# Optimization experiments

Hardware: AMD Instinct MI355X
Metric: run time of the kernel (lower is better)

## Reference

```python
import jax, jax.numpy as jnp
import numpy as np

N_NODES = 50000
N_GRAPHS = 250
NODES_PER_GRAPH = 200
EDGES_PER_GRAPH = 3200  # avg degree 16
F_IN = 128
EMB = 128
HID = 128
VOCAB = 1000
N_REL = 8


def setup_inputs() -> dict:
    key = jax.random.key(0)
    ks = jax.random.split(key, 16)

    # message: col 0 = discrete token id (stored as float), col 1 = continuous value
    disc = jax.random.randint(ks[0], (N_GRAPHS,), 0, VOCAB).astype(jnp.float32)
    cont = jax.random.normal(ks[1], (N_GRAPHS,), dtype=jnp.float32)
    message = jnp.stack([disc, cont], axis=1)  # [B, 2]

    x = jax.random.normal(ks[2], (N_NODES, F_IN), dtype=jnp.float32)

    # within-graph edges: local indices + per-graph node offset
    offs = (jnp.arange(N_GRAPHS, dtype=jnp.int64) * NODES_PER_GRAPH)[:, None]
    src = (jax.random.randint(ks[3], (N_GRAPHS, EDGES_PER_GRAPH), 0, NODES_PER_GRAPH) + offs).reshape(-1)
    dst = (jax.random.randint(ks[4], (N_GRAPHS, EDGES_PER_GRAPH), 0, NODES_PER_GRAPH) + offs).reshape(-1)
    edge_index = jnp.stack([src, dst], axis=0).astype(jnp.int64)  # [2, E]
    edge_type = jax.random.randint(ks[5], (N_GRAPHS * EDGES_PER_GRAPH,), 0, N_REL).astype(jnp.int64)

    batch = jnp.repeat(jnp.arange(N_GRAPHS, dtype=jnp.int64), NODES_PER_GRAPH)  # [N]

    s = 0.05
    W1 = jax.random.normal(ks[6], (N_REL, F_IN, EMB), dtype=jnp.float32) * s
    root1 = jax.random.normal(ks[7], (F_IN, EMB), dtype=jnp.float32) * s
    b1 = jnp.zeros((EMB,), dtype=jnp.float32)
    W2 = jax.random.normal(ks[8], (N_REL, EMB, EMB), dtype=jnp.float32) * s
    root2 = jax.random.normal(ks[9], (EMB, EMB), dtype=jnp.float32) * s
    b2 = jnp.zeros((EMB,), dtype=jnp.float32)
    embed_table = jax.random.normal(ks[10], (VOCAB, EMB), dtype=jnp.float32) * s
    cont_w = jax.random.normal(ks[11], (1, EMB), dtype=jnp.float32) * s
    cont_b = jnp.zeros((EMB,), dtype=jnp.float32)
    msg_w = jax.random.normal(ks[12], (2 * EMB, HID), dtype=jnp.float32) * s
    msg_b = jnp.zeros((HID,), dtype=jnp.float32)

    return {
        "message": message, "x": x, "edge_index": edge_index, "edge_type": edge_type,
        "batch": batch, "max_nodes": NODES_PER_GRAPH,
        "W1": W1, "root1": root1, "b1": b1, "W2": W2, "root2": root2, "b2": b2,
        "embed_table": embed_table, "cont_w": cont_w, "cont_b": cont_b,
        "msg_w": msg_w, "msg_b": msg_b,
    }


def _rgcn_conv(h, src, dst, edge_type, W, root, b, n_nodes, n_rel):
    # per-node per-relation transform, then gather per edge: avoids [E,F,F] weight gather
    hW = jnp.einsum('nf,rfo->nro', h, W)          # [N, R, O]
    msg = hW[src, edge_type]                       # [E, O]
    # mean aggregation per (dst, relation) as in PyG RGCNConv(aggr='mean')
    key_dr = dst * n_rel + edge_type
    cnt = jax.ops.segment_sum(jnp.ones_like(edge_type, dtype=h.dtype), key_dr,
                              num_segments=n_nodes * n_rel)
    norm = 1.0 / jnp.maximum(cnt[key_dr], 1.0)     # [E]
    agg = jax.ops.segment_sum(msg * norm[:, None], dst, num_segments=n_nodes)  # [N, O]
    return agg + h @ root + b


def reference(message, x, edge_index, edge_type, batch, max_nodes,
              W1, root1, b1, W2, root2, b2,
              embed_table, cont_w, cont_b, msg_w, msg_b):
    n_nodes = x.shape[0]
    n_rel = W1.shape[0]
    n_graphs = message.shape[0]
    src, dst = edge_index[0], edge_index[1]

    # --- RGCN node embeddings (2 layers, ReLU between) ---
    h = _rgcn_conv(x, src, dst, edge_type, W1, root1, b1, n_nodes, n_rel)
    h = jax.nn.relu(h)
    node_emb = _rgcn_conv(h, src, dst, edge_type, W2, root2, b2, n_nodes, n_rel)  # [N, EMB]

    # --- message representation ---
    disc_tok = message[:, 0].astype(jnp.int32)
    disc_emb = embed_table[disc_tok]                                   # [B, EMB]
    cont_emb = jax.nn.relu(message[:, 1:2] @ cont_w + cont_b)          # [B, EMB]
    combined = jnp.concatenate([disc_emb, cont_emb], axis=1)           # [B, 2*EMB]
    message_repr = jax.nn.relu(combined @ msg_w + msg_b)               # [B, HID]

    # --- per-node dot score against its graph's message, padded per graph ---
    scores = jnp.einsum('ne,ne->n', node_emb, message_repr[batch])     # [N]
    counts = jax.ops.segment_sum(jnp.ones((n_nodes,), dtype=jnp.int32), batch,
                                 num_segments=n_graphs)
    start = jnp.cumsum(counts) - counts                                # exclusive cumsum
    pos = jnp.arange(n_nodes) - start[batch]                           # slot within graph
    logits = jnp.full((n_graphs, max_nodes), -jnp.inf, dtype=scores.dtype)
    logits = logits.at[batch, pos].set(scores)
    return logits
```

## Files before the change

### kernel.cpp

```cpp
#include <hip/hip_runtime.h>
#include <stdint.h>

#define G_   250
#define P_   200
#define EPG  3200
#define E_   800000
#define F_   128
#define R_   8
#define HROW 136
#define NKEY (R_ * P_)
#define BSTG (8 * 4 * 64 * 8)

typedef _Float16 f16x8 __attribute__((ext_vector_type(8)));
typedef _Float16 f16x4 __attribute__((ext_vector_type(4)));
typedef float    f32x4 __attribute__((ext_vector_type(4)));
typedef float    f32x16 __attribute__((ext_vector_type(16)));

__global__ __launch_bounds__(256) void k_wstage(const float* __restrict__ W1, const float* __restrict__ root1,
                                                const float* __restrict__ W2, const float* __restrict__ root2,
                                                _Float16* __restrict__ wf) {
  int tt = blockIdx.x * 256 + threadIdx.x;
  int lane = tt & 63;
  int ntj  = (tt >> 6) & 3;
  int kt   = (tt >> 8) & 7;
  int rl   = tt >> 11;
  int r = rl % 9, l = rl / 9;
  const float* Wl = (l == 0) ? W1 : W2;
  const float* rt = (l == 0) ? root1 : root2;
  int kbase = kt * 16 + (lane >> 5) * 8;
  int n = ntj * 32 + (lane & 31);
  f16x8 v;
#pragma unroll
  for (int j = 0; j < 8; j++) {
    float f = (r < 8) ? Wl[(r * F_ + kbase + j) * F_ + n] : rt[(kbase + j) * F_ + n];
    v[j] = (_Float16)f;
  }
  *((f16x8*)(wf + (((rl * 8 + kt) * 4 + ntj) * 64 + lane) * 8)) = v;
}

__device__ __forceinline__ void gather_rel(f16x8 (&a)[8], const _Float16* __restrict__ Ap,
                                           const unsigned short* __restrict__ csr,
                                           const int* __restrict__ offs,
                                           int key, bool rowAct, int ck) {
  int o = 0, n = 0;
  if (rowAct) { o = offs[key]; n = offs[key + 1] - o; }
  f16x8 z = {0, 0, 0, 0, 0, 0, 0, 0};
#pragma unroll
  for (int kt = 0; kt < 8; kt++) a[kt] = z;
  int t = 0;
  for (; t + 2 <= n; t += 2) {
    int s0 = (int)csr[o + t];
    int s1 = (int)csr[o + t + 1];
    const _Float16* hp0 = &Ap[s0 * HROW + ck];
    const _Float16* hp1 = &Ap[s1 * HROW + ck];
    f16x8 u0[8], u1[8];
#pragma unroll
    for (int kt = 0; kt < 8; kt++) u0[kt] = *((const f16x8*)(hp0 + kt * 16));
#pragma unroll
    for (int kt = 0; kt < 8; kt++) u1[kt] = *((const f16x8*)(hp1 + kt * 16));
#pragma unroll
    for (int kt = 0; kt < 8; kt++) a[kt] += u0[kt] + u1[kt];
  }
  if (t < n) {
    int s0 = (int)csr[o + t];
    const _Float16* hp0 = &Ap[s0 * HROW + ck];
#pragma unroll
    for (int kt = 0; kt < 8; kt++) a[kt] += *((const f16x8*)(hp0 + kt * 16));
  }
  float nf = (n > 0) ? 1.0f / (float)n : 0.0f;
  _Float16 nh = (_Float16)nf;
#pragma unroll
  for (int kt = 0; kt < 8; kt++) a[kt] *= nh;
}

__device__ __forceinline__ void gather_root(f16x8 (&a)[8], const _Float16* __restrict__ Ap,
                                            int rowA, int ck) {
  const _Float16* hp = &Ap[rowA * HROW + ck];
#pragma unroll
  for (int kt = 0; kt < 8; kt++) a[kt] = *((const f16x8*)(hp + kt * 16));
}

__device__ __forceinline__ void mfma_rel(f32x16 (&acc)[4], const f16x8 (&a)[8],
                                         const _Float16* __restrict__ bp, int lane) {
  __builtin_amdgcn_s_setprio(1);
#pragma unroll
  for (int kt = 0; kt < 8; kt++) {
#pragma unroll
    for (int nt = 0; nt < 4; nt++) {
      f16x8 b = *((const f16x8*)&bp[((kt * 4 + nt) * 64 + lane) * 8]);
      acc[nt] = __builtin_amdgcn_mfma_f32_32x32x16_f16(a[kt], b, acc[nt], 0, 0, 0);
    }
  }
  __builtin_amdgcn_s_setprio(0);
}

__global__ __launch_bounds__(512, 1) void k_main(
    const float* __restrict__ x, const int* __restrict__ ei, const int* __restrict__ et,
    const _Float16* __restrict__ wf, const float* __restrict__ b1, const float* __restrict__ b2,
    const float* __restrict__ message, const float* __restrict__ embed,
    const float* __restrict__ cw, const float* __restrict__ cb,
    const float* __restrict__ mw, const float* __restrict__ mb,
    float* __restrict__ out) {
  __shared__ __attribute__((aligned(16))) _Float16 hbuf0[P_ * HROW];
  __shared__ __attribute__((aligned(16))) _Float16 hbuf1[P_ * HROW];
  __shared__ __attribute__((aligned(16))) _Float16 Bstage[BSTG];
  __shared__ unsigned short csrS[EPG];
  __shared__ int offsS[NKEY + 1];
  __shared__ float msgS[F_ + 1];

  int g = blockIdx.x, tid = threadIdx.x;
  int lane = tid & 63, wave = tid >> 6;
  int m32 = lane & 31, kh = lane >> 5;

  int*   Sint = (int*)hbuf1;
  int*   cnt  = Sint;
  int*   cur  = Sint + 1600;
  int*   eRec = Sint + 3200;
  float* comb = (float*)(Sint + 6400);
  float* red  = (float*)(Sint + 6656);

  f16x8 st0[4];
#pragma unroll
  for (int i = 0; i < 4; i++)
    st0[i] = *((const f16x8*)(wf + i * 4096 + tid * 8));

  for (int i = tid; i < P_ * 32; i += 512) {
    int row = i >> 5, c4 = i & 31;
    const float4 v = ((const float4*)x)[(g * P_ + row) * 32 + c4];
    f16x4 pk = { (_Float16)v.x, (_Float16)v.y, (_Float16)v.z, (_Float16)v.w };
    *((f16x4*)&hbuf0[row * HROW + c4 * 4]) = pk;
  }
  for (int i = tid; i < NKEY; i += 512) { cnt[i] = 0; cur[i] = 0; }
  if (tid < F_) {
    int tok = (int)message[g * 2];
    float cont = message[g * 2 + 1];
    comb[tid] = embed[tok * F_ + tid];
    float ce = cont * cw[tid] + cb[tid];
    comb[F_ + tid] = ce > 0.0f ? ce : 0.0f;
  }
#pragma unroll
  for (int i = 0; i < 4; i++)
    *((f16x8*)(Bstage + i * 4096 + tid * 8)) = st0[i];
  __syncthreads();

  int base = g * EPG, nbase = g * P_;
  if (wave < 6) {
    for (int e = wave * 64 + lane; e < EPG; e += 384) {
      int s = ei[base + e] - nbase;
      int d = ei[E_ + base + e] - nbase;
      int r = et[base + e];
      eRec[e] = s | (d << 8) | (r << 16);
      atomicAdd(&cnt[r * P_ + d], 1);
    }
  } else {
    int col = tid & 127;
    float acc = 0.0f;
#pragma unroll 16
    for (int k2 = 0; k2 < 256; k2++) acc += comb[k2] * mw[k2 * F_ + col];
    red[col] = acc;
  }
  __syncthreads();

  if (wave == 0) {
    int4 vv[8];
    int osum = 0;
    if (lane < 50) {
      const int4* cp = (const int4*)(cnt + lane * 32);
#pragma unroll
      for (int i = 0; i < 8; i++) { vv[i] = cp[i]; osum += vv[i].x + vv[i].y + vv[i].z + vv[i].w; }
    }
    int incl = osum;
#pragma unroll
    for (int d = 1; d < 64; d <<= 1) {
      int t2 = __shfl_up(incl, d, 64);
      if (lane >= d) incl += t2;
    }
    int run = incl - osum;
    if (lane < 50) {
#pragma unroll
      for (int i = 0; i < 8; i++) {
        offsS[lane * 32 + i * 4 + 0] = run; run += vv[i].x;
        offsS[lane * 32 + i * 4 + 1] = run; run += vv[i].y;
        offsS[lane * 32 + i * 4 + 2] = run; run += vv[i].z;
        offsS[lane * 32 + i * 4 + 3] = run; run += vv[i].w;
      }
    }
    if (lane == 0) offsS[NKEY] = EPG;
  } else if (wave == 1) {
    float m0 = mb[lane] + red[lane];
    float m1 = mb[lane + 64] + red[lane + 64];
    m0 = m0 > 0.0f ? m0 : 0.0f;
    m1 = m1 > 0.0f ? m1 : 0.0f;
    msgS[lane] = m0; msgS[lane + 64] = m1;
    float p = m0 * b2[lane] + m1 * b2[lane + 64];
#pragma unroll
    for (int d = 32; d > 0; d >>= 1) p += __shfl_xor(p, d, 64);
    if (lane == 0) msgS[F_] = p;
  }
  __syncthreads();

  for (int e = tid; e < EPG; e += 512) {
    int rec = eRec[e];
    int s = rec & 255, d = (rec >> 8) & 255, r = rec >> 16;
    int key = r * P_ + d;
    int pos = atomicAdd(&cur[key], 1);
    csrS[offsS[key] + pos] = (unsigned short)s;
  }
  __syncthreads();

  int jobBase = wave * 25;
  bool rowAct = (m32 < 25);
  int myD = jobBase + m32;
  int ck = kh * 8;
  int rowA = jobBase + (rowAct ? m32 : 24);

  for (int l = 0; l < 2; l++) {
    const _Float16* Ap = (l == 0) ? hbuf0 : hbuf1;
    _Float16* balt = (l == 0) ? hbuf1 : hbuf0;
    f32x16 acc[4];
#pragma unroll
    for (int nt = 0; nt < 4; nt++)
#pragma unroll
      for (int i = 0; i < 16; i++) acc[nt][i] = 0.0f;
    const _Float16* wl = wf + l * (9 * BSTG);

    f16x8 aA[8], aB[8];
    gather_rel(aA, Ap, csrS, offsS, 0 * P_ + myD, rowAct, ck);

    for (int p = 0; p < 4; p++) {
      int r1 = 2 * p + 1;
      f16x8 st2[4];
      {
        const _Float16* wn = wl + r1 * BSTG;
#pragma unroll
        for (int i = 0; i < 4; i++)
          st2[i] = *((const f16x8*)(wn + i * 4096 + tid * 8));
      }
      mfma_rel(acc, aA, Bstage, lane);
      gather_rel(aB, Ap, csrS, offsS, r1 * P_ + myD, rowAct, ck);
#pragma unroll
      for (int i = 0; i < 4; i++)
        *((f16x8*)(balt + i * 4096 + tid * 8)) = st2[i];
      __syncthreads();
      {
        const _Float16* wn = wl + (r1 + 1) * BSTG;
#pragma unroll
        for (int i = 0; i < 4; i++)
          st2[i] = *((const f16x8*)(wn + i * 4096 + tid * 8));
      }
      mfma_rel(acc, aB, balt, lane);
      if (p < 3)
        gather_rel(aA, Ap, csrS, offsS, (2 * p + 2) * P_ + myD, rowAct, ck);
      else
        gather_root(aA, Ap, rowA, ck);
#pragma unroll
      for (int i = 0; i < 4; i++)
        *((f16x8*)(Bstage + i * 4096 + tid * 8)) = st2[i];
      __syncthreads();
    }
    if (l == 0) {
      f16x8 st3[4];
      const _Float16* wn = wf + 9 * BSTG;
#pragma unroll
      for (int i = 0; i < 4; i++)
        st3[i] = *((const f16x8*)(wn + i * 4096 + tid * 8));
      mfma_rel(acc, aA, Bstage, lane);
      __syncthreads();
#pragma unroll
      for (int i = 0; i < 4; i++)
        *((f16x8*)(Bstage + i * 4096 + tid * 8)) = st3[i];
#pragma unroll
      for (int nt = 0; nt < 4; nt++) {
        int col = nt * 32 + m32;
        float bias = b1[col];
#pragma unroll
        for (int reg = 0; reg < 16; reg++) {
          int row = (reg & 3) + 8 * (reg >> 2) + 4 * kh;
          if (row < 25) {
            float v = acc[nt][reg] + bias;
            v = v > 0.0f ? v : 0.0f;
            hbuf1[(jobBase + row) * HROW + col] = (_Float16)v;
          }
        }
      }
      __syncthreads();
    } else {
      mfma_rel(acc, aA, Bstage, lane);
      float db2 = msgS[F_];
#pragma unroll
      for (int reg = 0; reg < 16; reg++) {
        int row = (reg & 3) + 8 * (reg >> 2) + 4 * kh;
        float p = 0.0f;
#pragma unroll
        for (int nt = 0; nt < 4; nt++)
          p += acc[nt][reg] * msgS[nt * 32 + m32];
        p += __shfl_xor(p, 16, 32);
        p += __shfl_xor(p, 8, 32);
        p += __shfl_xor(p, 4, 32);
        p += __shfl_xor(p, 2, 32);
        p += __shfl_xor(p, 1, 32);
        if (m32 == 0 && row < 25)
          out[g * P_ + jobBase + row] = p + db2;
      }
    }
  }
}

extern "C" void kernel_launch(void* const* d_in, const int* in_sizes, int n_in,
                              void* d_out, int out_size, void* d_ws, size_t ws_size,
                              hipStream_t stream) {
  const float* message = (const float*)d_in[0];
  const float* x       = (const float*)d_in[1];
  const int*   ei      = (const int*)d_in[2];
  const int*   et      = (const int*)d_in[3];
  const float* W1      = (const float*)d_in[6];
  const float* root1   = (const float*)d_in[7];
  const float* b1      = (const float*)d_in[8];
  const float* W2      = (const float*)d_in[9];
  const float* root2   = (const float*)d_in[10];
  const float* b2      = (const float*)d_in[11];
  const float* embed   = (const float*)d_in[12];
  const float* cw      = (const float*)d_in[13];
  const float* cb      = (const float*)d_in[14];
  const float* mw      = (const float*)d_in[15];
  const float* mb      = (const float*)d_in[16];

  _Float16* wfrag = (_Float16*)d_ws;
  float*    out   = (float*)d_out;

  hipLaunchKernelGGL(k_wstage, dim3(144), dim3(256), 0, stream, W1, root1, W2, root2, wfrag);
  hipLaunchKernelGGL(k_main, dim3(G_), dim3(512), 0, stream, x, ei, et, wfrag, b1, b2,
                     message, embed, cw, cb, mw, mb, out);
}
```

Baseline: 169.8 us.

## Read relation weight fragments directly from global instead of LDS staging

Drops the shared-memory double-buffered staging of per-relation weight tiles and the barriers that guarded it. The MFMA loop now loads B fragments straight from the pre-swizzled fp16 weight buffer in global memory, relying on the caches. This removes LDS stores and several __syncthreads per layer. In exchange, every wave issues its own global loads inside the MFMA loop, which adds cache traffic and exposes global-load latency that the staging used to hide.

```diff
diff --git a/kernel.cpp b/kernel.cpp
--- a/kernel.cpp
+++ b/kernel.cpp
@@ -80,14 +80,14 @@
   for (int kt = 0; kt < 8; kt++) a[kt] = *((const f16x8*)(hp + kt * 16));
 }
 
-__device__ __forceinline__ void mfma_rel(f32x16 (&acc)[4], const f16x8 (&a)[8],
-                                         const _Float16* __restrict__ bp, int lane) {
+__device__ __forceinline__ void mfma_relG(f32x16 (&acc)[4], const f16x8 (&a)[8],
+                                          const _Float16* __restrict__ wr, int lane) {
   __builtin_amdgcn_s_setprio(1);
 #pragma unroll
   for (int kt = 0; kt < 8; kt++) {
 #pragma unroll
     for (int nt = 0; nt < 4; nt++) {
-      f16x8 b = *((const f16x8*)&bp[((kt * 4 + nt) * 64 + lane) * 8]);
+      f16x8 b = *((const f16x8*)(wr + ((kt * 4 + nt) * 64 + lane) * 8));
       acc[nt] = __builtin_amdgcn_mfma_f32_32x32x16_f16(a[kt], b, acc[nt], 0, 0, 0);
     }
   }
@@ -103,7 +103,6 @@
     float* __restrict__ out) {
   __shared__ __attribute__((aligned(16))) _Float16 hbuf0[P_ * HROW];
   __shared__ __attribute__((aligned(16))) _Float16 hbuf1[P_ * HROW];
-  __shared__ __attribute__((aligned(16))) _Float16 Bstage[BSTG];
   __shared__ unsigned short csrS[EPG];
   __shared__ int offsS[NKEY + 1];
   __shared__ float msgS[F_ + 1];
@@ -118,11 +117,6 @@
   int*   eRec = Sint + 3200;
   float* comb = (float*)(Sint + 6400);
   float* red  = (float*)(Sint + 6656);
-
-  f16x8 st0[4];
-#pragma unroll
-  for (int i = 0; i < 4; i++)
-    st0[i] = *((const f16x8*)(wf + i * 4096 + tid * 8));
 
   for (int i = tid; i < P_ * 32; i += 512) {
     int row = i >> 5, c4 = i & 31;
@@ -138,9 +132,6 @@
     float ce = cont * cw[tid] + cb[tid];
     comb[F_ + tid] = ce > 0.0f ? ce : 0.0f;
   }
-#pragma unroll
-  for (int i = 0; i < 4; i++)
-    *((f16x8*)(Bstage + i * 4096 + tid * 8)) = st0[i];
   __syncthreads();
 
   int base = g * EPG, nbase = g * P_;
@@ -216,7 +207,6 @@
 
   for (int l = 0; l < 2; l++) {
     const _Float16* Ap = (l == 0) ? hbuf0 : hbuf1;
-    _Float16* balt = (l == 0) ? hbuf1 : hbuf0;
     f32x16 acc[4];
 #pragma unroll
     for (int nt = 0; nt < 4; nt++)
@@ -228,47 +218,17 @@
     gather_rel(aA, Ap, csrS, offsS, 0 * P_ + myD, rowAct, ck);
 
     for (int p = 0; p < 4; p++) {
-      int r1 = 2 * p + 1;
-      f16x8 st2[4];
-      {
-        const _Float16* wn = wl + r1 * BSTG;
-#pragma unroll
-        for (int i = 0; i < 4; i++)
-          st2[i] = *((const f16x8*)(wn + i * 4096 + tid * 8));
-      }
-      mfma_rel(acc, aA, Bstage, lane);
-      gather_rel(aB, Ap, csrS, offsS, r1 * P_ + myD, rowAct, ck);
-#pragma unroll
-      for (int i = 0; i < 4; i++)
-        *((f16x8*)(balt + i * 4096 + tid * 8)) = st2[i];
-      __syncthreads();
-      {
-        const _Float16* wn = wl + (r1 + 1) * BSTG;
-#pragma unroll
-        for (int i = 0; i < 4; i++)
-          st2[i] = *((const f16x8*)(wn + i * 4096 + tid * 8));
-      }
-      mfma_rel(acc, aB, balt, lane);
+      mfma_relG(acc, aA, wl + (2 * p) * BSTG, lane);
+      gather_rel(aB, Ap, csrS, offsS, (2 * p + 1) * P_ + myD, rowAct, ck);
+      mfma_relG(acc, aB, wl + (2 * p + 1) * BSTG, lane);
       if (p < 3)
         gather_rel(aA, Ap, csrS, offsS, (2 * p + 2) * P_ + myD, rowAct, ck);
       else
         gather_root(aA, Ap, rowA, ck);
-#pragma unroll
-      for (int i = 0; i < 4; i++)
-        *((f16x8*)(Bstage + i * 4096 + tid * 8)) = st2[i];
-      __syncthreads();
-    }
+    }
+    mfma_relG(acc, aA, wl + 8 * BSTG, lane);
+
     if (l == 0) {
-      f16x8 st3[4];
-      const _Float16* wn = wf + 9 * BSTG;
-#pragma unroll
-      for (int i = 0; i < 4; i++)
-        st3[i] = *((const f16x8*)(wn + i * 4096 + tid * 8));
-      mfma_rel(acc, aA, Bstage, lane);
-      __syncthreads();
-#pragma unroll
-      for (int i = 0; i < 4; i++)
-        *((f16x8*)(Bstage + i * 4096 + tid * 8)) = st3[i];
 #pragma unroll
       for (int nt = 0; nt < 4; nt++) {
         int col = nt * 32 + m32;
@@ -285,7 +245,6 @@
       }
       __syncthreads();
     } else {
-      mfma_rel(acc, aA, Bstage, lane);
       float db2 = msgS[F_];
 #pragma unroll
       for (int reg = 0; reg < 16; reg++) {
```

After: 208.1 us. +22.6%, slower.
